# Performance work log

Hardware: AMD Instinct MI355X
Metric: run time of the kernel (lower is better)

## Reference

```python
import jax, jax.numpy as jnp
import numpy as np

B, N, D, H = 4, 4096, 64, 128
N_STATES = 6
K = 10  # top-k nearest neighbors in detect_basins
EPS = 1e-12


def setup_inputs() -> dict:
    key = jax.random.key(0)
    ks = jax.random.split(key, 12)
    s = 0.05
    return {
        "conformations": jax.random.normal(ks[0], (B, N, D), dtype=jnp.float32),
        "native_state": jax.random.normal(ks[1], (B, D), dtype=jnp.float32),
        # energy net: D -> H -> H//2 -> 1
        "We1": jax.random.normal(ks[2], (D, H), dtype=jnp.float32) * s,
        "be1": jnp.zeros((H,), jnp.float32),
        "We2": jax.random.normal(ks[3], (H, H // 2), dtype=jnp.float32) * s,
        "be2": jnp.zeros((H // 2,), jnp.float32),
        "We3": jax.random.normal(ks[4], (H // 2, 1), dtype=jnp.float32) * s,
        "be3": jnp.zeros((1,), jnp.float32),
        # state classifier: D -> H -> 6
        "Ws1": jax.random.normal(ks[5], (D, H), dtype=jnp.float32) * s,
        "bs1": jnp.zeros((H,), jnp.float32),
        "Ws2": jax.random.normal(ks[6], (H, N_STATES), dtype=jnp.float32) * s,
        "bs2": jnp.zeros((N_STATES,), jnp.float32),
    }


def reference(conformations, native_state, We1, be1, We2, be2, We3, be3, Ws1, bs1, Ws2, bs2):
    relu = jax.nn.relu

    def analyze(conf, native):  # conf: (N, D), native: (D,)
        # predict_energy
        h = relu(conf @ We1 + be1)
        h = relu(h @ We2 + be2)
        e = (h @ We3 + be3)[:, 0]  # (N,)

        # detect_basins: pairwise euclidean distances via Gram trick
        sq = jnp.sum(conf * conf, axis=-1)  # (N,)
        d2 = sq[:, None] + sq[None, :] - 2.0 * (conf @ conf.T)
        dist = jnp.sqrt(jnp.clip(d2, EPS))  # (N, N); eps keeps sqrt grad finite at diag

        negv, idx = jax.lax.top_k(-dist, K)   # ascending distances; idx[:,0] == self
        r = -negv[:, -1]                      # k-th smallest distance per row
        neigh_e = e[idx[:, 1:]]               # (N, K-1) energies of 9 nearest neighbors
        is_basin = jnp.all(e[:, None] <= neigh_e, axis=1)  # local-minimum test

        mask = dist < r[:, None]              # points strictly inside basin radius (incl self)
        depth = jnp.max(jnp.where(mask, e[None, :], -jnp.inf), axis=1) - e
        width = jnp.sum(jnp.where(mask, dist, 0.0), axis=1) / jnp.sum(mask, axis=1)

        # classify_state (computed for every sample; original queries it per basin center)
        logits = relu(conf @ Ws1 + bs1) @ Ws2 + bs2  # (N, 6)

        # compute_funnel_metrics
        nd = jnp.sqrt(jnp.sum((conf - native) ** 2, axis=-1))  # (N,)
        native_energy = e[jnp.argmin(nd)]
        funnel_depth = jnp.max(e) - native_energy
        ruggedness = jnp.std(e, ddof=1)  # torch.std is unbiased
        corr = jnp.corrcoef(jnp.stack([nd, e]))[0, 1]
        se = e[jnp.argsort(nd)]
        frustration = jnp.mean((se[1:] > se[:-1]).astype(jnp.float32))
        metrics = jnp.stack([funnel_depth, ruggedness, corr, frustration, native_energy])
        return e, is_basin, depth, width, logits, metrics

    return jax.vmap(analyze)(conformations, native_state)
```

## Files before the change

### kernel.cpp

```cpp
#include <hip/hip_runtime.h>
#include <float.h>
#include <math.h>

#define NPTS 4096
#define NBATCH 4
#define BN (NBATCH * NPTS)
#define EPSC 1e-12f
#define JS 4
#define CSTRIDE 204
#define NT (NPTS / JS / 64)

typedef __attribute__((ext_vector_type(8))) short bfrag;
typedef __attribute__((ext_vector_type(4))) short bhalf;
typedef __attribute__((ext_vector_type(4))) float f32x4;

#define MFMA(A, B, C) __builtin_amdgcn_mfma_f32_16x16x32_bf16((A), (B), (C), 0, 0, 0)

__device__ __forceinline__ bool dless(float d1, int i1, float d2, int i2) {
  return (d1 < d2) || ((d1 == d2) && (i1 < i2));
}

__device__ __forceinline__ unsigned short f2bf(float x) {
  unsigned b = __float_as_uint(x);
  return (unsigned short)((b + 0x7FFFu + ((b >> 16) & 1u)) >> 16);
}
__device__ __forceinline__ float bf2f(unsigned short u) {
  return __uint_as_float(((unsigned)u) << 16);
}
__device__ __forceinline__ void bf3(float x, unsigned short& u0, unsigned short& u1,
                                    unsigned short& u2) {
  u0 = f2bf(x);
  float r = x - bf2f(u0);
  u1 = f2bf(r);
  r = r - bf2f(u1);
  u2 = f2bf(r);
}

__device__ __forceinline__ void cp16(const void* g, void* l) {
  __builtin_amdgcn_global_load_lds(
      (const __attribute__((address_space(1))) unsigned int*)g,
      (__attribute__((address_space(3))) unsigned int*)l, 16, 0, 0);
}
__device__ __forceinline__ void cp4(const void* g, void* l) {
  __builtin_amdgcn_global_load_lds(
      (const __attribute__((address_space(1))) unsigned int*)g,
      (__attribute__((address_space(3))) unsigned int*)l, 4, 0, 0);
}

__global__ __launch_bounds__(256) void bf3_kernel(
    const float* __restrict__ conf, unsigned short* __restrict__ cbf) {
  const int g = blockIdx.x * 256 + threadIdx.x;
  const int pt = g >> 4;
  const int k4 = (g & 15) << 2;
  float4 v = *(const float4*)(conf + (size_t)pt * 64 + k4);
  unsigned short x0, x1, x2, y0, y1, y2, z0, z1, z2, w0, w1, w2;
  bf3(v.x, x0, x1, x2);
  bf3(v.y, y0, y1, y2);
  bf3(v.z, z0, z1, z2);
  bf3(v.w, w0, w1, w2);
  unsigned short* dst = cbf + (size_t)pt * CSTRIDE + k4;
  *(bhalf*)&dst[0] = (bhalf){(short)x0, (short)y0, (short)z0, (short)w0};
  *(bhalf*)&dst[64] = (bhalf){(short)x1, (short)y1, (short)z1, (short)w1};
  *(bhalf*)&dst[128] = (bhalf){(short)x2, (short)y2, (short)z2, (short)w2};
}

__device__ __forceinline__ void gemm32x128(const float (*A)[64], const float* W,
                                           const float* bias, float (*O)[128], int tid) {
  const int pi = (tid >> 5) << 2;
  const int ci = (tid & 31) << 2;
  float acc[4][4] = {};
  for (int k0 = 0; k0 < 64; k0 += 4) {
    alignas(16) float av[4][4], wv[4][4];
#pragma unroll
    for (int r = 0; r < 4; ++r) *(float4*)av[r] = *(const float4*)&A[pi + r][k0];
#pragma unroll
    for (int kk = 0; kk < 4; ++kk) *(float4*)wv[kk] = *(const float4*)&W[(k0 + kk) * 128 + ci];
#pragma unroll
    for (int kk = 0; kk < 4; ++kk)
#pragma unroll
      for (int r = 0; r < 4; ++r)
#pragma unroll
        for (int c = 0; c < 4; ++c)
          acc[r][c] = fmaf(av[r][kk], wv[kk][c], acc[r][c]);
  }
#pragma unroll
  for (int r = 0; r < 4; ++r)
#pragma unroll
    for (int c = 0; c < 4; ++c)
      O[pi + r][ci + c] = fmaxf(acc[r][c] + bias[ci + c], 0.f);
}

__global__ __launch_bounds__(256) void mlp_kernel(
    const float* __restrict__ conf, const float* __restrict__ native,
    const float* __restrict__ We1, const float* __restrict__ be1,
    const float* __restrict__ We2, const float* __restrict__ be2,
    const float* __restrict__ We3, const float* __restrict__ be3,
    const float* __restrict__ Ws1, const float* __restrict__ bs1,
    const float* __restrict__ Ws2, const float* __restrict__ bs2,
    float* __restrict__ e_out, float* __restrict__ logits_out,
    float* __restrict__ sq_ws, float* __restrict__ nd_ws) {
  __shared__ __align__(16) float Wbuf[8192];
  __shared__ __align__(16) float confs[32][64];
  __shared__ __align__(16) float hbuf[32][128];
  __shared__ float nat[64];
  __shared__ float b1s[128], b2s[64], w3s[64], bs1s[128], ws2s[768], bs2s[6];
  __shared__ float be3s;

  const int tid = threadIdx.x;
  const int blk = blockIdx.x;
  const int b = blk >> 7;
  const int pbase = (blk & 127) * 32;
  const float* confb = conf + ((size_t)b * NPTS + pbase) * 64;

  for (int q = tid; q < 512; q += 256) {
    float4 v = *(const float4*)(confb + q * 4);
    *(float4*)&confs[q >> 4][(q & 15) << 2] = v;
  }
  if (tid < 64) nat[tid] = native[b * 64 + tid];
  if (tid < 128) b1s[tid] = be1[tid];
  if (tid < 64) b2s[tid] = be2[tid];
  if (tid < 64) w3s[tid] = We3[tid];
  if (tid < 128) bs1s[tid] = bs1[tid];
  for (int q = tid; q < 768; q += 256) ws2s[q] = Ws2[q];
  if (tid < 6) bs2s[tid] = bs2[tid];
  if (tid == 0) be3s = be3[0];
  for (int q = tid; q < 2048; q += 256)
    *(float4*)&Wbuf[q * 4] = *(const float4*)(Ws1 + q * 4);
  __syncthreads();

  if (tid < 32) {
    float rs_[8], rn_[8];
#pragma unroll
    for (int u = 0; u < 8; ++u) {
      float c = confs[tid][u];
      rs_[u] = c * c;
      float d = c - nat[u];
      rn_[u] = d * d;
    }
    for (int d0 = 8; d0 < 64; d0 += 8) {
#pragma unroll
      for (int u = 0; u < 8; ++u) {
        float c = confs[tid][d0 + u];
        rs_[u] += c * c;
        float d = c - nat[d0 + u];
        rn_[u] += d * d;
      }
    }
    float s = ((rs_[0] + rs_[1]) + (rs_[2] + rs_[3])) + ((rs_[4] + rs_[5]) + (rs_[6] + rs_[7]));
    float n = ((rn_[0] + rn_[1]) + (rn_[2] + rn_[3])) + ((rn_[4] + rn_[5]) + (rn_[6] + rn_[7]));
    sq_ws[(size_t)b * NPTS + pbase + tid] = s;
    nd_ws[(size_t)b * NPTS + pbase + tid] = sqrtf(n);
  }

  gemm32x128(confs, Wbuf, bs1s, hbuf, tid);
  __syncthreads();

  for (int q = tid; q < 2048; q += 256)
    *(float4*)&Wbuf[q * 4] = *(const float4*)(We1 + q * 4);
  if (tid < 192) {
    int p = tid / 6, s = tid % 6;
    float acc = 0.f;
#pragma unroll 8
    for (int h = 0; h < 128; ++h)
      acc = fmaf(hbuf[p][h], ws2s[h * 6 + s], acc);
    logits_out[((size_t)b * NPTS + pbase + p) * 6 + s] = acc + bs2s[s];
  }
  __syncthreads();

  gemm32x128(confs, Wbuf, b1s, hbuf, tid);
  __syncthreads();

  for (int q = tid; q < 2048; q += 256)
    *(float4*)&Wbuf[q * 4] = *(const float4*)(We2 + q * 4);
  __syncthreads();

  if (tid < 128) {
    const int pi = (tid >> 4) << 2;
    const int ci = (tid & 15) << 2;
    float acc[4][4] = {};
    for (int k0 = 0; k0 < 128; k0 += 4) {
      alignas(16) float av[4][4], wv[4][4];
#pragma unroll
      for (int r = 0; r < 4; ++r) *(float4*)av[r] = *(const float4*)&hbuf[pi + r][k0];
#pragma unroll
      for (int kk = 0; kk < 4; ++kk) *(float4*)wv[kk] = *(const float4*)&Wbuf[(k0 + kk) * 64 + ci];
#pragma unroll
      for (int kk = 0; kk < 4; ++kk)
#pragma unroll
        for (int r = 0; r < 4; ++r)
#pragma unroll
          for (int c = 0; c < 4; ++c)
            acc[r][c] = fmaf(av[r][kk], wv[kk][c], acc[r][c]);
    }
#pragma unroll
    for (int r = 0; r < 4; ++r)
#pragma unroll
      for (int c = 0; c < 4; ++c)
        confs[pi + r][ci + c] = fmaxf(acc[r][c] + b2s[ci + c], 0.f);
  }
  __syncthreads();

  if (tid < 32) {
    float acc = 0.f;
#pragma unroll
    for (int k = 0; k < 64; ++k)
      acc = fmaf(confs[tid][k], w3s[k], acc);
    e_out[(size_t)b * NPTS + pbase + tid] = acc + be3s;
  }
}

__device__ __forceinline__ bfrag ldfrag(const unsigned short* p) {
  bhalf lo = *(const bhalf*)p;
  bhalf hi = *(const bhalf*)(p + 4);
  return __builtin_shufflevector(lo, hi, 0, 1, 2, 3, 4, 5, 6, 7);
}

__device__ __forceinline__ void stage_async(const unsigned short* src,
                                            unsigned short* BU,
                                            const float* sqsrc, float* sqjs,
                                            int tid) {
  const char* s = (const char*)src;
  char* d = (char*)BU;
#pragma unroll
  for (int it = 0; it < 6; ++it) {
    const int q = it * 256 + tid;
    cp16(s + (size_t)q * 16, d + (size_t)q * 16);
  }
  if (tid < 96) {
    const int q = 1536 + tid;
    cp16(s + (size_t)q * 16, d + (size_t)q * 16);
  }
  if (tid < 64) cp4(sqsrc + tid, sqjs + tid);
}

__global__ __launch_bounds__(256, 1) void topk_part_kernel(
    const unsigned short* __restrict__ cbf, const float* __restrict__ sq_ws,
    float* __restrict__ topd, unsigned short* __restrict__ topi) {
  __shared__ __align__(16) unsigned short BU[64 * CSTRIDE];
  __shared__ __align__(16) float Dsf[64 * 68];
  __shared__ float sqjs[64];

  const int tid = threadIdx.x;
  const int b = blockIdx.z;
  const int i0 = blockIdx.x * 64;
  const int jbase = blockIdx.y * (NPTS / JS);
  const unsigned short* cbfb = cbf + (size_t)b * NPTS * CSTRIDE;
  const float* sqb = sq_ws + (size_t)b * NPTS;

  const int l = tid & 63, w = tid >> 6;
  const int cl = l & 15, g = l >> 4;

  const unsigned short* arow = cbfb + (size_t)(i0 + 16 * w + cl) * CSTRIDE + g * 8;
  const bfrag a00 = ldfrag(arow + 0);
  const bfrag a01 = ldfrag(arow + 32);
  const bfrag a10 = ldfrag(arow + 64);
  const bfrag a11 = ldfrag(arow + 96);
  const bfrag a20 = ldfrag(arow + 128);
  const bfrag a21 = ldfrag(arow + 160);
  float sqar[4];
#pragma unroll
  for (int e = 0; e < 4; ++e) sqar[e] = sqb[i0 + 16 * w + 4 * g + e];

  const int irow = tid >> 2, q4 = tid & 3;

  unsigned long long lk[10];
#pragma unroll
  for (int k = 0; k < 10; ++k) lk[k] = 0x7F7FFFFF7FFFFFFFULL;
  float thrf = FLT_MAX;

  stage_async(cbfb + (size_t)jbase * CSTRIDE, BU, sqb + jbase, sqjs, tid);
  __syncthreads();

  for (int jt = 0; jt < NT; ++jt) {
    const int j0 = jbase + jt * 64;

#pragma unroll
    for (int c = 0; c < 4; ++c) {
      const unsigned short* bp = &BU[(16 * c + cl) * CSTRIDE + g * 8];
      const bfrag b00 = ldfrag(bp + 0);
      const bfrag b01 = ldfrag(bp + 32);
      const bfrag b10 = ldfrag(bp + 64);
      const bfrag b11 = ldfrag(bp + 96);
      const bfrag b20 = ldfrag(bp + 128);
      const bfrag b21 = ldfrag(bp + 160);
      f32x4 acc = {0.f, 0.f, 0.f, 0.f};
      acc = MFMA(a00, b00, acc); acc = MFMA(a01, b01, acc);
      acc = MFMA(a00, b10, acc); acc = MFMA(a01, b11, acc);
      acc = MFMA(a10, b00, acc); acc = MFMA(a11, b01, acc);
      acc = MFMA(a00, b20, acc); acc = MFMA(a01, b21, acc);
      acc = MFMA(a10, b10, acc); acc = MFMA(a11, b11, acc);
      acc = MFMA(a20, b00, acc); acc = MFMA(a21, b01, acc);
      const int col = 16 * c + cl;
      const float sj = sqjs[col];
#pragma unroll
      for (int e = 0; e < 4; ++e) {
        const int rw = 16 * w + 4 * g + e;
        float d2 = fmaf(-2.f, acc[e], sqar[e] + sj);
        Dsf[rw * 68 + col] = fmaxf(d2, EPSC);
      }
    }
    __syncthreads();

    if (jt + 1 < NT)
      stage_async(cbfb + (size_t)(j0 + 64) * CSTRIDE, BU, sqb + j0 + 64, sqjs, tid);

    const float* drow = &Dsf[irow * 68 + q4 * 16];
    unsigned mask = 0;
#pragma unroll
    for (int cc = 0; cc < 4; ++cc) {
      float4 v = *(const float4*)&drow[cc * 4];
      mask |= (v.x <= thrf) ? (1u << (cc * 4 + 0)) : 0u;
      mask |= (v.y <= thrf) ? (1u << (cc * 4 + 1)) : 0u;
      mask |= (v.z <= thrf) ? (1u << (cc * 4 + 2)) : 0u;
      mask |= (v.w <= thrf) ? (1u << (cc * 4 + 3)) : 0u;
    }
    const int cnt = __popc(mask);
    int K = cnt;
#pragma unroll
    for (int off = 32; off >= 1; off >>= 1) K = max(K, __shfl_xor(K, off, 64));
    for (int k = 0; k < K; ++k) {
      int id = (__ffs(mask) - 1) & 15;
      mask &= mask - 1;
      const bool act = (k < cnt);
      const float d = drow[id];
      if (act) {
        unsigned long long cur =
            (((unsigned long long)__float_as_uint(d)) << 32) |
            (unsigned long long)(unsigned)(j0 + q4 * 16 + id);
        if (cur < lk[9]) {
#pragma unroll
          for (int kk = 0; kk < 10; ++kk) {
            bool lt = cur < lk[kk];
            unsigned long long mn = lt ? cur : lk[kk];
            cur = lt ? lk[kk] : cur;
            lk[kk] = mn;
          }
        }
      }
    }

    float t = __uint_as_float((unsigned)(lk[9] >> 32));
    t = fminf(t, __shfl_xor(t, 1, 4));
    t = fminf(t, __shfl_xor(t, 2, 4));
    thrf = t;
    __syncthreads();
  }

  float* mrgD = Dsf;
  int* mrgI = (int*)BU;
  {
#pragma unroll
    for (int k = 0; k < 10; ++k) {
      mrgD[irow * 40 + q4 * 10 + k] = __uint_as_float((unsigned)(lk[k] >> 32));
      mrgI[irow * 40 + q4 * 10 + k] = (int)(unsigned)(lk[k] & 0xFFFFFFFFu);
    }
  }
  __syncthreads();
  if (tid < 64) {
    const int base = tid * 40;
    int h0 = 0, h1 = 0, h2 = 0, h3 = 0;
    const size_t obase = (((size_t)b * NPTS + i0 + tid) * JS + blockIdx.y) * 10;
    for (int k = 0; k < 10; ++k) {
      float bd = FLT_MAX; int bi = 0x7fffffff; int bl = -1;
      { float d = mrgD[base + h0];      int ii = mrgI[base + h0];      if (dless(d, ii, bd, bi)) { bd = d; bi = ii; bl = 0; } }
      { float d = mrgD[base + 10 + h1]; int ii = mrgI[base + 10 + h1]; if (dless(d, ii, bd, bi)) { bd = d; bi = ii; bl = 1; } }
      { float d = mrgD[base + 20 + h2]; int ii = mrgI[base + 20 + h2]; if (dless(d, ii, bd, bi)) { bd = d; bi = ii; bl = 2; } }
      { float d = mrgD[base + 30 + h3]; int ii = mrgI[base + 30 + h3]; if (dless(d, ii, bd, bi)) { bd = d; bi = ii; bl = 3; } }
      h0 += (bl == 0); h1 += (bl == 1); h2 += (bl == 2); h3 += (bl == 3);
      topd[obase + k] = bd;
      topi[obase + k] = (unsigned short)bi;
    }
  }
}

__global__ __launch_bounds__(256) void topk_merge_kernel(
    const float* __restrict__ topd, const unsigned short* __restrict__ topi,
    const float* __restrict__ e_in, float* __restrict__ basin_out,
    float* __restrict__ depth_out, float* __restrict__ width_out) {
  const int g = blockIdx.x * 256 + threadIdx.x;
  const int b = g >> 12;
  const float* eb = e_in + (size_t)b * NPTS;
  const float* td = topd + (size_t)g * (JS * 10);
  const unsigned short* ti = topi + (size_t)g * (JS * 10);
  const float e_i = eb[g & (NPTS - 1)];
  int h0 = 0, h1 = 0, h2 = 0, h3 = 0;
  float dk[10];
  int ik[10];
#pragma unroll
  for (int k = 0; k < 10; ++k) {
    float bd = FLT_MAX; int bi = 0x7fffffff; int bl = -1;
    { float d = td[h0];      int ii = ti[h0];      if (dless(d, ii, bd, bi)) { bd = d; bi = ii; bl = 0; } }
    { float d = td[10 + h1]; int ii = ti[10 + h1]; if (dless(d, ii, bd, bi)) { bd = d; bi = ii; bl = 1; } }
    { float d = td[20 + h2]; int ii = ti[20 + h2]; if (dless(d, ii, bd, bi)) { bd = d; bi = ii; bl = 2; } }
    { float d = td[30 + h3]; int ii = ti[30 + h3]; if (dless(d, ii, bd, bi)) { bd = d; bi = ii; bl = 3; } }
    h0 += (bl == 0); h1 += (bl == 1); h2 += (bl == 2); h3 += (bl == 3);
    dk[k] = bd;
    ik[k] = bi;
  }
  const float r2 = dk[9];
  bool basin = true;
  float mx = -FLT_MAX, sum = 0.f, cnt = 0.f;
#pragma unroll
  for (int k = 0; k < 10; ++k) {
    float ev = eb[ik[k]];
    if (dk[k] < r2) { mx = fmaxf(mx, ev); sum += sqrtf(dk[k]); cnt += 1.f; }
    if (k >= 1) basin = basin && (e_i <= ev);
  }
  basin_out[g] = basin ? 1.f : 0.f;
  depth_out[g] = mx - e_i;
  width_out[g] = sum / cnt;
}

__global__ __launch_bounds__(256) void rank_kernel(
    const float* __restrict__ nd_ws, const float* __restrict__ e_in,
    float* __restrict__ se_ws) {
  __shared__ __align__(16) float ndl[4096];
  const int tid = threadIdx.x;
  const int b = blockIdx.y;
  const int i0 = blockIdx.x * 64;
  const float* ndb = nd_ws + (size_t)b * NPTS;
  for (int q = tid; q < 1024; q += 256)
    *(float4*)&ndl[q * 4] = *(const float4*)(ndb + q * 4);
  __syncthreads();
  const int i = i0 + (tid >> 2);
  const int qp = tid & 3;
  const float ndi = ndl[i];
  int rank = 0;
  for (int j = qp * 1024; j < qp * 1024 + 1024; j += 4) {
    float4 v = *(const float4*)&ndl[j];
    rank += (v.x < ndi) || (v.x == ndi && (j + 0) < i);
    rank += (v.y < ndi) || (v.y == ndi && (j + 1) < i);
    rank += (v.z < ndi) || (v.z == ndi && (j + 2) < i);
    rank += (v.w < ndi) || (v.w == ndi && (j + 3) < i);
  }
  rank += __shfl_xor(rank, 1, 4);
  rank += __shfl_xor(rank, 2, 4);
  if (qp == 0) se_ws[(size_t)b * NPTS + rank] = e_in[(size_t)b * NPTS + i];
}

__device__ __forceinline__ float block_sum(float v, float* red, int tid) {
  red[tid] = v;
  __syncthreads();
  for (int s = 512; s > 0; s >>= 1) {
    if (tid < s) red[tid] += red[tid + s];
    __syncthreads();
  }
  float r = red[0];
  __syncthreads();
  return r;
}
__device__ __forceinline__ float block_max(float v, float* red, int tid) {
  red[tid] = v;
  __syncthreads();
  for (int s = 512; s > 0; s >>= 1) {
    if (tid < s) red[tid] = fmaxf(red[tid], red[tid + s]);
    __syncthreads();
  }
  float r = red[0];
  __syncthreads();
  return r;
}

__global__ __launch_bounds__(1024) void metrics_kernel(
    const float* __restrict__ e_in, const float* __restrict__ nd_ws,
    const float* __restrict__ se_ws, float* __restrict__ metrics_out) {
  __shared__ __align__(16) float el[4096], ndl[4096], sel[4096];
  __shared__ float red[1024];
  __shared__ int redi[1024];
  const int tid = threadIdx.x;
  const int b = blockIdx.x;
  const float* eb = e_in + (size_t)b * NPTS;
  const float* ndb = nd_ws + (size_t)b * NPTS;
  const float* seb = se_ws + (size_t)b * NPTS;
  *(float4*)&el[tid * 4] = *(const float4*)(eb + tid * 4);
  *(float4*)&ndl[tid * 4] = *(const float4*)(ndb + tid * 4);
  *(float4*)&sel[tid * 4] = *(const float4*)(seb + tid * 4);
  __syncthreads();

  float pe = 0.f, pnd = 0.f;
  for (int p = tid; p < 4096; p += 1024) { pe += el[p]; pnd += ndl[p]; }
  float me = block_sum(pe, red, tid) / 4096.f;
  float mnd = block_sum(pnd, red, tid) / 4096.f;

  float sxx = 0.f, syy = 0.f, sxy = 0.f, mx = -FLT_MAX;
  float bestv = FLT_MAX;
  int besti = 0x7fffffff;
  for (int p = tid; p < 4096; p += 1024) {
    float de = el[p] - me, dn = ndl[p] - mnd;
    syy += de * de;
    sxx += dn * dn;
    sxy += de * dn;
    mx = fmaxf(mx, el[p]);
    if (ndl[p] < bestv || (ndl[p] == bestv && p < besti)) { bestv = ndl[p]; besti = p; }
  }
  float fr = 0.f;
  for (int p = tid; p < 4095; p += 1024) fr += (sel[p + 1] > sel[p]) ? 1.f : 0.f;

  sxx = block_sum(sxx, red, tid);
  syy = block_sum(syy, red, tid);
  sxy = block_sum(sxy, red, tid);
  mx = block_max(mx, red, tid);
  fr = block_sum(fr, red, tid);

  red[tid] = bestv;
  redi[tid] = besti;
  __syncthreads();
  for (int s = 512; s > 0; s >>= 1) {
    if (tid < s) {
      float ov = red[tid + s];
      int oi = redi[tid + s];
      if (ov < red[tid] || (ov == red[tid] && oi < redi[tid])) { red[tid] = ov; redi[tid] = oi; }
    }
    __syncthreads();
  }
  if (tid == 0) {
    float ne = el[redi[0]];
    metrics_out[b * 5 + 0] = mx - ne;
    metrics_out[b * 5 + 1] = sqrtf(syy / 4095.f);
    metrics_out[b * 5 + 2] = sxy / sqrtf(sxx * syy);
    metrics_out[b * 5 + 3] = fr / 4095.f;
    metrics_out[b * 5 + 4] = ne;
  }
}

extern "C" void kernel_launch(void* const* d_in, const int* in_sizes, int n_in,
                              void* d_out, int out_size, void* d_ws, size_t ws_size,
                              hipStream_t stream) {
  const float* conf = (const float*)d_in[0];
  const float* native = (const float*)d_in[1];
  const float* We1 = (const float*)d_in[2];
  const float* be1 = (const float*)d_in[3];
  const float* We2 = (const float*)d_in[4];
  const float* be2 = (const float*)d_in[5];
  const float* We3 = (const float*)d_in[6];
  const float* be3 = (const float*)d_in[7];
  const float* Ws1 = (const float*)d_in[8];
  const float* bs1 = (const float*)d_in[9];
  const float* Ws2 = (const float*)d_in[10];
  const float* bs2 = (const float*)d_in[11];

  float* out = (float*)d_out;
  float* e_out = out;
  float* basin_out = out + BN;
  float* depth_out = out + 2 * BN;
  float* width_out = out + 3 * BN;
  float* logits_out = out + 4 * BN;
  float* metrics_out = out + 10 * BN;

  float* wsf = (float*)d_ws;
  float* sq_ws = wsf;
  float* nd_ws = wsf + BN;
  float* se_ws = wsf + 2 * (size_t)BN;
  float* topd = wsf + 3 * (size_t)BN;
  unsigned short* topi = (unsigned short*)(wsf + 43 * (size_t)BN);
  unsigned short* cbf = (unsigned short*)(wsf + 63 * (size_t)BN);

  bf3_kernel<<<dim3(BN * 16 / 256), dim3(256), 0, stream>>>(conf, cbf);
  mlp_kernel<<<dim3(512), dim3(256), 0, stream>>>(
      conf, native, We1, be1, We2, be2, We3, be3, Ws1, bs1, Ws2, bs2,
      e_out, logits_out, sq_ws, nd_ws);
  topk_part_kernel<<<dim3(64, JS, NBATCH), dim3(256), 0, stream>>>(
      cbf, sq_ws, topd, topi);
  topk_merge_kernel<<<dim3(BN / 256), dim3(256), 0, stream>>>(
      topd, topi, e_out, basin_out, depth_out, width_out);
  rank_kernel<<<dim3(64, NBATCH), dim3(256), 0, stream>>>(nd_ws, e_out, se_ws);
  metrics_kernel<<<dim3(NBATCH), dim3(1024), 0, stream>>>(e_out, nd_ws, se_ws, metrics_out);
}
```

Baseline: 237.9 us.

## Fuse bf16 split into MLP, merge top-k merge with rank, use wave reductions

```diff
diff --git a/kernel.cpp b/kernel.cpp
--- a/kernel.cpp
+++ b/kernel.cpp
@@ -45,23 +45,6 @@
   __builtin_amdgcn_global_load_lds(
       (const __attribute__((address_space(1))) unsigned int*)g,
       (__attribute__((address_space(3))) unsigned int*)l, 4, 0, 0);
-}
-
-__global__ __launch_bounds__(256) void bf3_kernel(
-    const float* __restrict__ conf, unsigned short* __restrict__ cbf) {
-  const int g = blockIdx.x * 256 + threadIdx.x;
-  const int pt = g >> 4;
-  const int k4 = (g & 15) << 2;
-  float4 v = *(const float4*)(conf + (size_t)pt * 64 + k4);
-  unsigned short x0, x1, x2, y0, y1, y2, z0, z1, z2, w0, w1, w2;
-  bf3(v.x, x0, x1, x2);
-  bf3(v.y, y0, y1, y2);
-  bf3(v.z, z0, z1, z2);
-  bf3(v.w, w0, w1, w2);
-  unsigned short* dst = cbf + (size_t)pt * CSTRIDE + k4;
-  *(bhalf*)&dst[0] = (bhalf){(short)x0, (short)y0, (short)z0, (short)w0};
-  *(bhalf*)&dst[64] = (bhalf){(short)x1, (short)y1, (short)z1, (short)w1};
-  *(bhalf*)&dst[128] = (bhalf){(short)x2, (short)y2, (short)z2, (short)w2};
 }
 
 __device__ __forceinline__ void gemm32x128(const float (*A)[64], const float* W,
@@ -98,7 +81,8 @@
     const float* __restrict__ Ws1, const float* __restrict__ bs1,
     const float* __restrict__ Ws2, const float* __restrict__ bs2,
     float* __restrict__ e_out, float* __restrict__ logits_out,
-    float* __restrict__ sq_ws, float* __restrict__ nd_ws) {
+    float* __restrict__ sq_ws, float* __restrict__ nd_ws,
+    unsigned short* __restrict__ cbf) {
   __shared__ __align__(16) float Wbuf[8192];
   __shared__ __align__(16) float confs[32][64];
   __shared__ __align__(16) float hbuf[32][128];
@@ -127,6 +111,20 @@
   for (int q = tid; q < 2048; q += 256)
     *(float4*)&Wbuf[q * 4] = *(const float4*)(Ws1 + q * 4);
   __syncthreads();
+
+  for (int q = tid; q < 512; q += 256) {
+    const int pl = q >> 4, k4 = (q & 15) << 2;
+    float4 v = *(const float4*)&confs[pl][k4];
+    unsigned short x0, x1, x2, y0, y1, y2, z0, z1, z2, w0, w1, w2;
+    bf3(v.x, x0, x1, x2);
+    bf3(v.y, y0, y1, y2);
+    bf3(v.z, z0, z1, z2);
+    bf3(v.w, w0, w1, w2);
+    unsigned short* dst = cbf + (size_t)(b * NPTS + pbase + pl) * CSTRIDE + k4;
+    *(bhalf*)&dst[0] = (bhalf){(short)x0, (short)y0, (short)z0, (short)w0};
+    *(bhalf*)&dst[64] = (bhalf){(short)x1, (short)y1, (short)z1, (short)w1};
+    *(bhalf*)&dst[128] = (bhalf){(short)x2, (short)y2, (short)z2, (short)w2};
+  }
 
   if (tid < 32) {
     float rs_[8], rn_[8];
@@ -318,15 +316,20 @@
     int K = cnt;
 #pragma unroll
     for (int off = 32; off >= 1; off >>= 1) K = max(K, __shfl_xor(K, off, 64));
+
+    int id = (__ffs(mask) - 1) & 15;
+    mask &= mask - 1;
+    float dcur = drow[id];
+    int jcur = j0 + q4 * 16 + id;
     for (int k = 0; k < K; ++k) {
-      int id = (__ffs(mask) - 1) & 15;
+      const int idn = (__ffs(mask) - 1) & 15;
       mask &= mask - 1;
-      const bool act = (k < cnt);
-      const float d = drow[id];
-      if (act) {
+      const float dnx = drow[idn];
+      const int jnx = j0 + q4 * 16 + idn;
+      if (k < cnt) {
         unsigned long long cur =
-            (((unsigned long long)__float_as_uint(d)) << 32) |
-            (unsigned long long)(unsigned)(j0 + q4 * 16 + id);
+            (((unsigned long long)__float_as_uint(dcur)) << 32) |
+            (unsigned long long)(unsigned)jcur;
         if (cur < lk[9]) {
 #pragma unroll
           for (int kk = 0; kk < 10; ++kk) {
@@ -337,6 +340,8 @@
           }
         }
       }
+      dcur = dnx;
+      jcur = jnx;
     }
 
     float t = __uint_as_float((unsigned)(lk[9] >> 32));
@@ -373,102 +378,91 @@
   }
 }
 
-__global__ __launch_bounds__(256) void topk_merge_kernel(
+__global__ __launch_bounds__(256) void merge_rank_kernel(
     const float* __restrict__ topd, const unsigned short* __restrict__ topi,
-    const float* __restrict__ e_in, float* __restrict__ basin_out,
-    float* __restrict__ depth_out, float* __restrict__ width_out) {
-  const int g = blockIdx.x * 256 + threadIdx.x;
-  const int b = g >> 12;
-  const float* eb = e_in + (size_t)b * NPTS;
-  const float* td = topd + (size_t)g * (JS * 10);
-  const unsigned short* ti = topi + (size_t)g * (JS * 10);
-  const float e_i = eb[g & (NPTS - 1)];
-  int h0 = 0, h1 = 0, h2 = 0, h3 = 0;
-  float dk[10];
-  int ik[10];
-#pragma unroll
-  for (int k = 0; k < 10; ++k) {
-    float bd = FLT_MAX; int bi = 0x7fffffff; int bl = -1;
-    { float d = td[h0];      int ii = ti[h0];      if (dless(d, ii, bd, bi)) { bd = d; bi = ii; bl = 0; } }
-    { float d = td[10 + h1]; int ii = ti[10 + h1]; if (dless(d, ii, bd, bi)) { bd = d; bi = ii; bl = 1; } }
-    { float d = td[20 + h2]; int ii = ti[20 + h2]; if (dless(d, ii, bd, bi)) { bd = d; bi = ii; bl = 2; } }
-    { float d = td[30 + h3]; int ii = ti[30 + h3]; if (dless(d, ii, bd, bi)) { bd = d; bi = ii; bl = 3; } }
-    h0 += (bl == 0); h1 += (bl == 1); h2 += (bl == 2); h3 += (bl == 3);
-    dk[k] = bd;
-    ik[k] = bi;
-  }
-  const float r2 = dk[9];
-  bool basin = true;
-  float mx = -FLT_MAX, sum = 0.f, cnt = 0.f;
-#pragma unroll
-  for (int k = 0; k < 10; ++k) {
-    float ev = eb[ik[k]];
-    if (dk[k] < r2) { mx = fmaxf(mx, ev); sum += sqrtf(dk[k]); cnt += 1.f; }
-    if (k >= 1) basin = basin && (e_i <= ev);
-  }
-  basin_out[g] = basin ? 1.f : 0.f;
-  depth_out[g] = mx - e_i;
-  width_out[g] = sum / cnt;
-}
-
-__global__ __launch_bounds__(256) void rank_kernel(
-    const float* __restrict__ nd_ws, const float* __restrict__ e_in,
-    float* __restrict__ se_ws) {
+    const float* __restrict__ e_in, const float* __restrict__ nd_ws,
+    float* __restrict__ basin_out, float* __restrict__ depth_out,
+    float* __restrict__ width_out, float* __restrict__ se_ws) {
   __shared__ __align__(16) float ndl[4096];
   const int tid = threadIdx.x;
-  const int b = blockIdx.y;
-  const int i0 = blockIdx.x * 64;
-  const float* ndb = nd_ws + (size_t)b * NPTS;
-  for (int q = tid; q < 1024; q += 256)
-    *(float4*)&ndl[q * 4] = *(const float4*)(ndb + q * 4);
-  __syncthreads();
-  const int i = i0 + (tid >> 2);
-  const int qp = tid & 3;
-  const float ndi = ndl[i];
-  int rank = 0;
-  for (int j = qp * 1024; j < qp * 1024 + 1024; j += 4) {
-    float4 v = *(const float4*)&ndl[j];
-    rank += (v.x < ndi) || (v.x == ndi && (j + 0) < i);
-    rank += (v.y < ndi) || (v.y == ndi && (j + 1) < i);
-    rank += (v.z < ndi) || (v.z == ndi && (j + 2) < i);
-    rank += (v.w < ndi) || (v.w == ndi && (j + 3) < i);
-  }
-  rank += __shfl_xor(rank, 1, 4);
-  rank += __shfl_xor(rank, 2, 4);
-  if (qp == 0) se_ws[(size_t)b * NPTS + rank] = e_in[(size_t)b * NPTS + i];
-}
-
-__device__ __forceinline__ float block_sum(float v, float* red, int tid) {
-  red[tid] = v;
-  __syncthreads();
-  for (int s = 512; s > 0; s >>= 1) {
-    if (tid < s) red[tid] += red[tid + s];
+  if (blockIdx.x < 64) {
+    const int g = blockIdx.x * 256 + tid;
+    const int b = g >> 12;
+    const float* eb = e_in + (size_t)b * NPTS;
+    const float* td = topd + (size_t)g * (JS * 10);
+    const unsigned short* ti = topi + (size_t)g * (JS * 10);
+    const float e_i = eb[g & (NPTS - 1)];
+    int h0 = 0, h1 = 0, h2 = 0, h3 = 0;
+    float dk[10];
+    int ik[10];
+#pragma unroll
+    for (int k = 0; k < 10; ++k) {
+      float bd = FLT_MAX; int bi = 0x7fffffff; int bl = -1;
+      { float d = td[h0];      int ii = ti[h0];      if (dless(d, ii, bd, bi)) { bd = d; bi = ii; bl = 0; } }
+      { float d = td[10 + h1]; int ii = ti[10 + h1]; if (dless(d, ii, bd, bi)) { bd = d; bi = ii; bl = 1; } }
+      { float d = td[20 + h2]; int ii = ti[20 + h2]; if (dless(d, ii, bd, bi)) { bd = d; bi = ii; bl = 2; } }
+      { float d = td[30 + h3]; int ii = ti[30 + h3]; if (dless(d, ii, bd, bi)) { bd = d; bi = ii; bl = 3; } }
+      h0 += (bl == 0); h1 += (bl == 1); h2 += (bl == 2); h3 += (bl == 3);
+      dk[k] = bd;
+      ik[k] = bi;
+    }
+    const float r2 = dk[9];
+    bool basin = true;
+    float mx = -FLT_MAX, sum = 0.f, cnt = 0.f;
+#pragma unroll
+    for (int k = 0; k < 10; ++k) {
+      float ev = eb[ik[k]];
+      if (dk[k] < r2) { mx = fmaxf(mx, ev); sum += sqrtf(dk[k]); cnt += 1.f; }
+      if (k >= 1) basin = basin && (e_i <= ev);
+    }
+    basin_out[g] = basin ? 1.f : 0.f;
+    depth_out[g] = mx - e_i;
+    width_out[g] = sum / cnt;
+  } else {
+    const int rb = blockIdx.x - 64;
+    const int b = rb >> 6;
+    const int i0 = (rb & 63) * 64;
+    const float* ndb = nd_ws + (size_t)b * NPTS;
+    for (int q = tid; q < 1024; q += 256)
+      *(float4*)&ndl[q * 4] = *(const float4*)(ndb + q * 4);
     __syncthreads();
-  }
-  float r = red[0];
-  __syncthreads();
-  return r;
-}
-__device__ __forceinline__ float block_max(float v, float* red, int tid) {
-  red[tid] = v;
-  __syncthreads();
-  for (int s = 512; s > 0; s >>= 1) {
-    if (tid < s) red[tid] = fmaxf(red[tid], red[tid + s]);
-    __syncthreads();
-  }
-  float r = red[0];
-  __syncthreads();
-  return r;
+    const int i = i0 + (tid >> 2);
+    const int qp = tid & 3;
+    const float ndi = ndl[i];
+    int rank = 0;
+    for (int j = qp * 1024; j < qp * 1024 + 1024; j += 4) {
+      float4 v = *(const float4*)&ndl[j];
+      rank += (v.x < ndi) || (v.x == ndi && (j + 0) < i);
+      rank += (v.y < ndi) || (v.y == ndi && (j + 1) < i);
+      rank += (v.z < ndi) || (v.z == ndi && (j + 2) < i);
+      rank += (v.w < ndi) || (v.w == ndi && (j + 3) < i);
+    }
+    rank += __shfl_xor(rank, 1, 4);
+    rank += __shfl_xor(rank, 2, 4);
+    if (qp == 0) se_ws[(size_t)b * NPTS + rank] = e_in[(size_t)b * NPTS + i];
+  }
+}
+
+__device__ __forceinline__ float wave_sum(float v) {
+#pragma unroll
+  for (int off = 32; off >= 1; off >>= 1) v += __shfl_xor(v, off, 64);
+  return v;
+}
+__device__ __forceinline__ float wave_max(float v) {
+#pragma unroll
+  for (int off = 32; off >= 1; off >>= 1) v = fmaxf(v, __shfl_xor(v, off, 64));
+  return v;
 }
 
 __global__ __launch_bounds__(1024) void metrics_kernel(
     const float* __restrict__ e_in, const float* __restrict__ nd_ws,
     const float* __restrict__ se_ws, float* __restrict__ metrics_out) {
   __shared__ __align__(16) float el[4096], ndl[4096], sel[4096];
-  __shared__ float red[1024];
-  __shared__ int redi[1024];
+  __shared__ float rA[16], rB[16], rC[16], rD[16], rE[16], rF[16], rV[16];
+  __shared__ int rI[16];
   const int tid = threadIdx.x;
   const int b = blockIdx.x;
+  const int wid = tid >> 6, ln = tid & 63;
   const float* eb = e_in + (size_t)b * NPTS;
   const float* ndb = nd_ws + (size_t)b * NPTS;
   const float* seb = se_ws + (size_t)b * NPTS;
@@ -479,8 +473,15 @@
 
   float pe = 0.f, pnd = 0.f;
   for (int p = tid; p < 4096; p += 1024) { pe += el[p]; pnd += ndl[p]; }
-  float me = block_sum(pe, red, tid) / 4096.f;
-  float mnd = block_sum(pnd, red, tid) / 4096.f;
+  pe = wave_sum(pe);
+  pnd = wave_sum(pnd);
+  if (ln == 0) { rA[wid] = pe; rB[wid] = pnd; }
+  __syncthreads();
+  float me = 0.f, mnd = 0.f;
+  for (int i = 0; i < 16; ++i) { me += rA[i]; mnd += rB[i]; }
+  me /= 4096.f;
+  mnd /= 4096.f;
+  __syncthreads();
 
   float sxx = 0.f, syy = 0.f, sxy = 0.f, mx = -FLT_MAX;
   float bestv = FLT_MAX;
@@ -496,29 +497,36 @@
   float fr = 0.f;
   for (int p = tid; p < 4095; p += 1024) fr += (sel[p + 1] > sel[p]) ? 1.f : 0.f;
 
-  sxx = block_sum(sxx, red, tid);
-  syy = block_sum(syy, red, tid);
-  sxy = block_sum(sxy, red, tid);
-  mx = block_max(mx, red, tid);
-  fr = block_sum(fr, red, tid);
-
-  red[tid] = bestv;
-  redi[tid] = besti;
-  __syncthreads();
-  for (int s = 512; s > 0; s >>= 1) {
-    if (tid < s) {
-      float ov = red[tid + s];
-      int oi = redi[tid + s];
-      if (ov < red[tid] || (ov == red[tid] && oi < redi[tid])) { red[tid] = ov; redi[tid] = oi; }
-    }
-    __syncthreads();
-  }
+  sxx = wave_sum(sxx);
+  syy = wave_sum(syy);
+  sxy = wave_sum(sxy);
+  mx = wave_max(mx);
+  fr = wave_sum(fr);
+#pragma unroll
+  for (int off = 32; off >= 1; off >>= 1) {
+    float ov = __shfl_xor(bestv, off, 64);
+    int oi = __shfl_xor(besti, off, 64);
+    if (ov < bestv || (ov == bestv && oi < besti)) { bestv = ov; besti = oi; }
+  }
+  if (ln == 0) {
+    rA[wid] = sxx; rB[wid] = syy; rC[wid] = sxy;
+    rD[wid] = mx;  rE[wid] = fr;  rV[wid] = bestv; rI[wid] = besti;
+  }
+  __syncthreads();
   if (tid == 0) {
-    float ne = el[redi[0]];
-    metrics_out[b * 5 + 0] = mx - ne;
-    metrics_out[b * 5 + 1] = sqrtf(syy / 4095.f);
-    metrics_out[b * 5 + 2] = sxy / sqrtf(sxx * syy);
-    metrics_out[b * 5 + 3] = fr / 4095.f;
+    float tsxx = 0.f, tsyy = 0.f, tsxy = 0.f, tmx = -FLT_MAX, tfr = 0.f;
+    float bv = FLT_MAX;
+    int bi = 0x7fffffff;
+    for (int i = 0; i < 16; ++i) {
+      tsxx += rA[i]; tsyy += rB[i]; tsxy += rC[i];
+      tmx = fmaxf(tmx, rD[i]); tfr += rE[i];
+      if (rV[i] < bv || (rV[i] == bv && rI[i] < bi)) { bv = rV[i]; bi = rI[i]; }
+    }
+    float ne = el[bi];
+    metrics_out[b * 5 + 0] = tmx - ne;
+    metrics_out[b * 5 + 1] = sqrtf(tsyy / 4095.f);
+    metrics_out[b * 5 + 2] = tsxy / sqrtf(tsxx * tsyy);
+    metrics_out[b * 5 + 3] = tfr / 4095.f;
     metrics_out[b * 5 + 4] = ne;
   }
 }
@@ -555,14 +563,12 @@
   unsigned short* topi = (unsigned short*)(wsf + 43 * (size_t)BN);
   unsigned short* cbf = (unsigned short*)(wsf + 63 * (size_t)BN);
 
-  bf3_kernel<<<dim3(BN * 16 / 256), dim3(256), 0, stream>>>(conf, cbf);
   mlp_kernel<<<dim3(512), dim3(256), 0, stream>>>(
       conf, native, We1, be1, We2, be2, We3, be3, Ws1, bs1, Ws2, bs2,
-      e_out, logits_out, sq_ws, nd_ws);
+      e_out, logits_out, sq_ws, nd_ws, cbf);
   topk_part_kernel<<<dim3(64, JS, NBATCH), dim3(256), 0, stream>>>(
       cbf, sq_ws, topd, topi);
-  topk_merge_kernel<<<dim3(BN / 256), dim3(256), 0, stream>>>(
-      topd, topi, e_out, basin_out, depth_out, width_out);
-  rank_kernel<<<dim3(64, NBATCH), dim3(256), 0, stream>>>(nd_ws, e_out, se_ws);
+  merge_rank_kernel<<<dim3(320), dim3(256), 0, stream>>>(
+      topd, topi, e_out, nd_ws, basin_out, depth_out, width_out, se_ws);
   metrics_kernel<<<dim3(NBATCH), dim3(1024), 0, stream>>>(e_out, nd_ws, se_ws, metrics_out);
 }
```

Measured after the change: 197.0 us. 17.2% less time.
